# Kernel tuning notes

Measured on AMD Instinct MI355X. Metric: run time of the kernel, lower is better.

The kernel has to match this reference:

```python
import jax, jax.numpy as jnp
import numpy as np

N_EMBD = 1024
HEAD_SIZE = 128
B, T = 8, 2048


def apply_rope(x):
    # x: (B, T, D); rotate interleaved pairs, matching torch view(B,T,D//2,2)
    b, t, d = x.shape
    freqs = 1.0 / (10000.0 ** (jnp.arange(0, d, 2, dtype=jnp.float32) / d))  # (D//2,)
    angles = jnp.arange(t, dtype=jnp.float32)[:, None] * freqs[None, :]      # (T, D//2)
    cos_a = jnp.cos(angles).astype(x.dtype)
    sin_a = jnp.sin(angles).astype(x.dtype)
    xr = x.reshape(b, t, d // 2, 2)
    x0, x1 = xr[..., 0], xr[..., 1]
    rot = jnp.stack([x0 * cos_a - x1 * sin_a, x0 * sin_a + x1 * cos_a], axis=-1)
    return rot.reshape(b, t, d)


def setup_inputs() -> dict:
    key = jax.random.key(0)
    kx, kq, kk, kv = jax.random.split(key, 4)
    x = jax.random.normal(kx, (B, T, N_EMBD), dtype=jnp.float32)
    scale = 0.02
    Wq = jax.random.normal(kq, (N_EMBD, HEAD_SIZE), dtype=jnp.float32) * scale
    Wk = jax.random.normal(kk, (N_EMBD, HEAD_SIZE), dtype=jnp.float32) * scale
    Wv = jax.random.normal(kv, (N_EMBD, HEAD_SIZE), dtype=jnp.float32) * scale
    return {"x": x, "Wq": Wq, "Wk": Wk, "Wv": Wv}


def reference(x, Wq, Wk, Wv):
    # QKV projections (bias=False)
    q = x @ Wq  # (B, T, H)
    k = x @ Wk
    v = x @ Wv
    q = apply_rope(q)
    k = apply_rope(k)
    d = k.shape[-1]
    wei = jnp.einsum('bqd,bkd->bqk', q, k) * (d ** -0.5)  # (B, T, T)
    causal = jnp.tril(jnp.ones((q.shape[1], q.shape[1]), dtype=bool))
    wei = jnp.where(causal, wei, jnp.finfo(wei.dtype).min)
    wei = jax.nn.softmax(wei, axis=-1)
    out = jnp.einsum('bqk,bkd->bqd', wei, v)  # (B, T, H)
    return out
```

## Files before the change

kernel.cpp:

```cpp
#include <hip/hip_runtime.h>
#include <math.h>

#define BB 8
#define TT 2048
#define EE 1024
#define DD 128

typedef _Float16 f16x8 __attribute__((ext_vector_type(8)));
typedef _Float16 f16x4 __attribute__((ext_vector_type(4)));
typedef float    f32x4 __attribute__((ext_vector_type(4)));
typedef float    f32x16 __attribute__((ext_vector_type(16)));

#define QSCALE 0.12752406f

__global__ __launch_bounds__(256)
void wt_prep_kernel(const float* __restrict__ Wq,
                    const float* __restrict__ Wk,
                    const float* __restrict__ Wv,
                    _Float16* __restrict__ Wt)
{
    const int n = blockIdx.x;
    const int m = n >> 7;
    const float* __restrict__ W = (m == 0) ? Wq : (m == 1) ? Wk : Wv;
    const int nl = n & 127;
#pragma unroll
    for (int j = 0; j < 4; j++) {
        int kk = threadIdx.x + 256 * j;
        Wt[(size_t)n * EE + kk] = (_Float16)W[(size_t)kk * DD + nl];
    }
}

__global__ __launch_bounds__(512)
void proj_rope_kernel(const float* __restrict__ x,
                      const _Float16* __restrict__ Wt,
                      _Float16* __restrict__ qh,
                      _Float16* __restrict__ kh,
                      _Float16* __restrict__ vt)
{
    const int r0   = blockIdx.x * 64;
    const int tid  = threadIdx.x;
    const int wave = tid >> 6;
    const int lane = tid & 63;
    const int half = lane >> 5;
    const int col  = lane & 31;
    const int wave_m = wave & 1;
    const int wave_n = wave >> 1;

    __shared__ _Float16 Xs[64][72];
    __shared__ _Float16 Ws[384][72];
    __shared__ _Float16 Out[64][136];

    f32x16 acc[3];
#pragma unroll
    for (int s = 0; s < 3; s++) acc[s] = (f32x16)0.f;

    const int xrow = tid >> 3, xc8 = (tid & 7) * 8;

    float4 xa0, xa1;
    f16x8  wv[6];
    {
        const float* p = &x[(size_t)(r0 + xrow) * EE + xc8];
        xa0 = *(const float4*)p;
        xa1 = *(const float4*)(p + 4);
#pragma unroll
        for (int j = 0; j < 6; j++) {
            int ch = tid + 512 * j;
            int nn = ch >> 3, cw = (ch & 7) * 8;
            wv[j] = *(const f16x8*)&Wt[(size_t)nn * EE + cw];
        }
    }

    for (int it = 0; it < 16; it++) {
        __syncthreads();
        {
            f16x8 h = { (_Float16)xa0.x, (_Float16)xa0.y, (_Float16)xa0.z, (_Float16)xa0.w,
                        (_Float16)xa1.x, (_Float16)xa1.y, (_Float16)xa1.z, (_Float16)xa1.w };
            *(f16x8*)&Xs[xrow][xc8] = h;
#pragma unroll
            for (int j = 0; j < 6; j++) {
                int ch = tid + 512 * j;
                int nn = ch >> 3, cw = (ch & 7) * 8;
                *(f16x8*)&Ws[nn][cw] = wv[j];
            }
        }
        if (it + 1 < 16) {
            int k0 = (it + 1) * 64;
            const float* p = &x[(size_t)(r0 + xrow) * EE + k0 + xc8];
            xa0 = *(const float4*)p;
            xa1 = *(const float4*)(p + 4);
#pragma unroll
            for (int j = 0; j < 6; j++) {
                int ch = tid + 512 * j;
                int nn = ch >> 3, cw = (ch & 7) * 8;
                wv[j] = *(const f16x8*)&Wt[(size_t)nn * EE + k0 + cw];
            }
        }
        __syncthreads();
#pragma unroll
        for (int kc = 0; kc < 4; kc++) {
            f16x8 afr = *(f16x8*)&Xs[wave_m * 32 + col][kc * 16 + half * 8];
#pragma unroll
            for (int s = 0; s < 3; s++) {
                f16x8 bfr = *(f16x8*)&Ws[wave_n * 96 + s * 32 + col][kc * 16 + half * 8];
                acc[s] = __builtin_amdgcn_mfma_f32_32x32x16_f16(afr, bfr, acc[s], 0, 0, 0);
            }
        }
    }

    const int bidx = r0 >> 11;
    const int t0   = r0 & (TT - 1);

    for (int p = 0; p < 3; p++) {
        __syncthreads();
#pragma unroll
        for (int s = 0; s < 3; s++) {
            int gs = wave_n * 3 + s;
            if ((gs >> 2) != p) continue;
            int dcol = (gs & 3) * 32 + col;
            float f = 0.f;
            if (p < 2)
                f = __powf(10000.0f, -(float)(dcol & ~1) * (1.0f / 128.0f));
#pragma unroll
            for (int rg = 0; rg < 16; rg++) {
                int mrow = wave_m * 32 + (rg & 3) + 8 * (rg >> 2) + 4 * half;
                float av = acc[s][rg];
                float res;
                if (p < 2) {
                    float ap = __shfl_xor(av, 1);
                    float sa, ca;
                    __sincosf((float)(t0 + mrow) * f, &sa, &ca);
                    res = av * ca + ap * ((dcol & 1) ? sa : -sa);
                    if (p == 0) res *= QSCALE;
                } else {
                    res = av;
                }
                Out[mrow][dcol] = (_Float16)res;
            }
        }
        __syncthreads();
        if (p < 2) {
            _Float16* __restrict__ dst = ((p == 0) ? qh : kh) + (size_t)r0 * DD;
#pragma unroll
            for (int j = 0; j < 2; j++) {
                int cidx = tid + 512 * j;
                int row = cidx >> 4, o = cidx & 15;
                *(f16x8*)&dst[(size_t)row * DD + o * 8] = *(f16x8*)&Out[row][o * 8];
            }
        } else {
#pragma unroll
            for (int j = 0; j < 2; j++) {
                int u = tid + 512 * j;
                int d = u >> 3, tg = u & 7;
                f16x8 vv;
#pragma unroll
                for (int e = 0; e < 8; e++) vv[e] = Out[tg * 8 + e][d];
                *(f16x8*)&vt[((size_t)(bidx * DD + d)) * TT + t0 + tg * 8] = vv;
            }
        }
    }
}

__global__ __launch_bounds__(256)
void attn_kernel(const _Float16* __restrict__ qh,
                 const _Float16* __restrict__ kh,
                 const _Float16* __restrict__ vth,
                 _Float16* __restrict__ opart,
                 float* __restrict__ mpart,
                 float* __restrict__ lpart)
{
    const int b  = blockIdx.y;
    const int v_ = 39 - blockIdx.x;
    int xt, c;
    if (v_ < 4)       { xt = v_;                  c = 0; }
    else if (v_ < 12) { xt = 4 + ((v_ - 4) >> 1); c = (v_ - 4) & 1; }
    else if (v_ < 24) { xt = 8 + (v_ - 12) / 3;   c = (v_ - 12) % 3; }
    else              { xt = 12 + ((v_ - 24) >> 2); c = (v_ - 24) & 3; }
    const int q0 = xt * 128;
    const int nt = 2 * xt + 2;
    const int kt_begin = c * 8;
    const int kt_end   = (kt_begin + 8 < nt) ? (kt_begin + 8) : nt;

    const int tid  = threadIdx.x;
    const int wave = tid >> 6;
    const int lane = tid & 63;
    const int half = lane >> 5;
    const int col  = lane & 31;

    __shared__ _Float16 Ks[64][136];
    __shared__ _Float16 Vt[128][72];
    __shared__ _Float16 Ps[4][32][72];

    const int qg = q0 + wave * 32 + col;
    f16x8 qb[8];
#pragma unroll
    for (int kc = 0; kc < 8; kc++)
        qb[kc] = *(const f16x8*)&qh[((size_t)b * TT + qg) * DD + kc * 16 + half * 8];

    f32x16 Of[4];
#pragma unroll
    for (int t = 0; t < 4; t++) Of[t] = (f32x16)0.f;
    float m_ = -1e30f, l_ = 0.f;

    f16x8 kr[4], vr[4];
    {
        const int kb0 = kt_begin * 64;
#pragma unroll
        for (int i = 0; i < 4; i++) {
            int idx = i * 256 + tid;
            int key = idx >> 4, cc = idx & 15;
            kr[i] = *(const f16x8*)&kh[((size_t)b * TT + kb0 + key) * DD + cc * 8];
        }
#pragma unroll
        for (int i = 0; i < 4; i++) {
            int idx = i * 256 + tid;
            int d = idx >> 3, cc = idx & 7;
            vr[i] = *(const f16x8*)&vth[((size_t)b * DD + d) * TT + kb0 + cc * 8];
        }
    }

    for (int kt = kt_begin; kt < kt_end; kt++) {
        const int kb0 = kt * 64;
        __syncthreads();
#pragma unroll
        for (int i = 0; i < 4; i++) {
            int idx = i * 256 + tid;
            int key = idx >> 4, cc = idx & 15;
            *(f16x8*)&Ks[key][cc * 8] = kr[i];
        }
#pragma unroll
        for (int i = 0; i < 4; i++) {
            int idx = i * 256 + tid;
            int d = idx >> 3, cc = idx & 7;
            *(f16x8*)&Vt[d][cc * 8] = vr[i];
        }
        if (kt + 1 < kt_end) {
            const int kb1 = kb0 + 64;
#pragma unroll
            for (int i = 0; i < 4; i++) {
                int idx = i * 256 + tid;
                int key = idx >> 4, cc = idx & 15;
                kr[i] = *(const f16x8*)&kh[((size_t)b * TT + kb1 + key) * DD + cc * 8];
            }
#pragma unroll
            for (int i = 0; i < 4; i++) {
                int idx = i * 256 + tid;
                int d = idx >> 3, cc = idx & 7;
                vr[i] = *(const f16x8*)&vth[((size_t)b * DD + d) * TT + kb1 + cc * 8];
            }
        }
        __syncthreads();

        f32x16 sf[2];
#pragma unroll
        for (int g = 0; g < 2; g++) {
            sf[g] = (f32x16)0.f;
#pragma unroll
            for (int kc = 0; kc < 8; kc++) {
                f16x8 kf = *(f16x8*)&Ks[g * 32 + col][kc * 16 + half * 8];
                sf[g] = __builtin_amdgcn_mfma_f32_32x32x16_f16(kf, qb[kc], sf[g], 0, 0, 0);
            }
        }

        const bool diag = (kt >= 2 * xt);
        float mloc = -1e30f;
#pragma unroll
        for (int g = 0; g < 2; g++)
#pragma unroll
            for (int rg = 0; rg < 16; rg++) {
                int key = kb0 + g * 32 + (rg & 3) + 8 * (rg >> 2) + 4 * half;
                float val = sf[g][rg];
                val = (!diag || key <= qg) ? val : -1e30f;
                sf[g][rg] = val;
                mloc = fmaxf(mloc, val);
            }
        mloc = fmaxf(mloc, __shfl_xor(mloc, 32));
        float mnew  = fmaxf(m_, mloc);
        float alpha = __builtin_amdgcn_exp2f(m_ - mnew);
        float ps = 0.f;
#pragma unroll
        for (int g = 0; g < 2; g++) {
#pragma unroll
            for (int rc = 0; rc < 4; rc++) {
                f16x4 p4;
#pragma unroll
                for (int rr = 0; rr < 4; rr++) {
                    float p = __builtin_amdgcn_exp2f(sf[g][4 * rc + rr] - mnew);
                    ps += p;
                    p4[rr] = (_Float16)p;
                }
                *(f16x4*)&Ps[wave][col][g * 32 + 8 * rc + 4 * half] = p4;
            }
        }
        ps += __shfl_xor(ps, 32);
        l_ = l_ * alpha + ps;
        m_ = mnew;
#pragma unroll
        for (int t = 0; t < 4; t++) Of[t] *= alpha;

        f16x8 pb[4];
#pragma unroll
        for (int kc = 0; kc < 4; kc++)
            pb[kc] = *(f16x8*)&Ps[wave][col][kc * 16 + half * 8];
#pragma unroll
        for (int t = 0; t < 4; t++) {
#pragma unroll
            for (int kc = 0; kc < 4; kc++) {
                f16x8 vf = *(f16x8*)&Vt[t * 32 + col][kc * 16 + half * 8];
                Of[t] = __builtin_amdgcn_mfma_f32_32x32x16_f16(vf, pb[kc], Of[t], 0, 0, 0);
            }
        }
    }

    const int slot = (b * 16 + xt) * 4 + c;
    _Float16* op = opart + ((size_t)slot * 128 + wave * 32 + col) * DD;
#pragma unroll
    for (int t = 0; t < 4; t++) {
#pragma unroll
        for (int rc = 0; rc < 4; rc++) {
            f16x4 o4 = { (_Float16)Of[t][4 * rc + 0], (_Float16)Of[t][4 * rc + 1],
                         (_Float16)Of[t][4 * rc + 2], (_Float16)Of[t][4 * rc + 3] };
            *(f16x4*)&op[t * 32 + 8 * rc + 4 * half] = o4;
        }
    }
    if (half == 0) {
        mpart[slot * 128 + wave * 32 + col] = m_;
        lpart[slot * 128 + wave * 32 + col] = l_;
    }
}

__global__ __launch_bounds__(256)
void combine_kernel(const _Float16* __restrict__ opart,
                    const float* __restrict__ mpart,
                    const float* __restrict__ lpart,
                    float* __restrict__ out)
{
    int gid = blockIdx.x * 256 + threadIdx.x;
    int d   = gid & 127;
    int t   = gid >> 7;
    int b   = t >> 11;
    int tl  = t & (TT - 1);
    int xt  = tl >> 7;
    int rl  = tl & 127;
    int np  = (2 * xt + 2 + 7) >> 3;
    int sb  = (b * 16 + xt) * 4;

    float mm = -1e30f;
    for (int j = 0; j < np; j++)
        mm = fmaxf(mm, mpart[(sb + j) * 128 + rl]);
    float acc = 0.f, den = 0.f;
    for (int j = 0; j < np; j++) {
        float w = __builtin_amdgcn_exp2f(mpart[(sb + j) * 128 + rl] - mm);
        den += w * lpart[(sb + j) * 128 + rl];
        acc += w * (float)opart[((size_t)(sb + j) * 128 + rl) * DD + d];
    }
    out[gid] = acc / den;
}

extern "C" void kernel_launch(void* const* d_in, const int* in_sizes, int n_in,
                              void* d_out, int out_size, void* d_ws, size_t ws_size,
                              hipStream_t stream)
{
    const float* x  = (const float*)d_in[0];
    const float* Wq = (const float*)d_in[1];
    const float* Wk = (const float*)d_in[2];
    const float* Wv = (const float*)d_in[3];
    float* out = (float*)d_out;

    const size_t NTOK = (size_t)BB * TT;
    _Float16* qh = (_Float16*)d_ws;
    _Float16* kh = qh + NTOK * DD;
    _Float16* vt = kh + NTOK * DD;
    _Float16* Wt = vt + NTOK * DD;
    _Float16* opart = Wt + (size_t)384 * EE;
    float* mp = (float*)(opart + (size_t)512 * 128 * DD);
    float* lp = mp + 512 * 128;

    wt_prep_kernel<<<dim3(384), dim3(256), 0, stream>>>(Wq, Wk, Wv, Wt);
    proj_rope_kernel<<<dim3(256), dim3(512), 0, stream>>>(x, Wt, qh, kh, vt);
    attn_kernel<<<dim3(40, BB), dim3(256), 0, stream>>>(qh, kh, vt, opart, mp, lp);
    combine_kernel<<<dim3((int)(NTOK * DD / 256)), dim3(256), 0, stream>>>(opart, mp, lp, out);
}
```

Baseline: 184.5 us.

## Pre-swizzle Q/K/V and weights into MFMA fragment order, drop LDS staging

Weights, Q, K and V are written in a layout that matches the MFMA operand fragments, so each lane can load its f16x8 fragment straight from global memory. This removes the shared-memory tiles and their barriers in both the projection and attention kernels. The cost is that K/V reuse across the 4 waves now depends on L1/L2 cache instead of LDS, with more global load traffic per block. Register prefetch pipelining is also gone, so load latency may be exposed.

```diff
diff --git a/kernel.cpp b/kernel.cpp
--- a/kernel.cpp
+++ b/kernel.cpp
@@ -13,29 +13,35 @@
 
 #define QSCALE 0.12752406f
 
+
 __global__ __launch_bounds__(256)
 void wt_prep_kernel(const float* __restrict__ Wq,
                     const float* __restrict__ Wk,
                     const float* __restrict__ Wv,
-                    _Float16* __restrict__ Wt)
-{
-    const int n = blockIdx.x;
-    const int m = n >> 7;
-    const float* __restrict__ W = (m == 0) ? Wq : (m == 1) ? Wk : Wv;
-    const int nl = n & 127;
-#pragma unroll
-    for (int j = 0; j < 4; j++) {
-        int kk = threadIdx.x + 256 * j;
-        Wt[(size_t)n * EE + kk] = (_Float16)W[(size_t)kk * DD + nl];
-    }
+                    _Float16* __restrict__ Wb)
+{
+    int gid = blockIdx.x * 256 + threadIdx.x;
+    int kc  = gid / 768;
+    int rem = gid - kc * 768;
+    int ns  = rem >> 6;
+    int ln  = rem & 63;
+    int n   = ns * 32 + (ln & 31);
+    int k0  = kc * 16 + (ln >> 5) * 8;
+    const float* __restrict__ W = (n < 128) ? Wq : (n < 256) ? Wk : Wv;
+    int nl = n & 127;
+    f16x8 w;
+#pragma unroll
+    for (int j = 0; j < 8; j++)
+        w[j] = (_Float16)W[(size_t)(k0 + j) * DD + nl];
+    *(f16x8*)&Wb[(size_t)gid * 8] = w;
 }
 
 __global__ __launch_bounds__(512)
 void proj_rope_kernel(const float* __restrict__ x,
-                      const _Float16* __restrict__ Wt,
-                      _Float16* __restrict__ qh,
-                      _Float16* __restrict__ kh,
-                      _Float16* __restrict__ vt)
+                      const _Float16* __restrict__ Wb,
+                      _Float16* __restrict__ Qb,
+                      _Float16* __restrict__ Ka,
+                      _Float16* __restrict__ Va)
 {
     const int r0   = blockIdx.x * 64;
     const int tid  = threadIdx.x;
@@ -46,64 +52,25 @@
     const int wave_m = wave & 1;
     const int wave_n = wave >> 1;
 
-    __shared__ _Float16 Xs[64][72];
-    __shared__ _Float16 Ws[384][72];
     __shared__ _Float16 Out[64][136];
 
     f32x16 acc[3];
 #pragma unroll
     for (int s = 0; s < 3; s++) acc[s] = (f32x16)0.f;
 
-    const int xrow = tid >> 3, xc8 = (tid & 7) * 8;
-
-    float4 xa0, xa1;
-    f16x8  wv[6];
-    {
-        const float* p = &x[(size_t)(r0 + xrow) * EE + xc8];
-        xa0 = *(const float4*)p;
-        xa1 = *(const float4*)(p + 4);
-#pragma unroll
-        for (int j = 0; j < 6; j++) {
-            int ch = tid + 512 * j;
-            int nn = ch >> 3, cw = (ch & 7) * 8;
-            wv[j] = *(const f16x8*)&Wt[(size_t)nn * EE + cw];
-        }
-    }
-
-    for (int it = 0; it < 16; it++) {
-        __syncthreads();
-        {
-            f16x8 h = { (_Float16)xa0.x, (_Float16)xa0.y, (_Float16)xa0.z, (_Float16)xa0.w,
-                        (_Float16)xa1.x, (_Float16)xa1.y, (_Float16)xa1.z, (_Float16)xa1.w };
-            *(f16x8*)&Xs[xrow][xc8] = h;
-#pragma unroll
-            for (int j = 0; j < 6; j++) {
-                int ch = tid + 512 * j;
-                int nn = ch >> 3, cw = (ch & 7) * 8;
-                *(f16x8*)&Ws[nn][cw] = wv[j];
-            }
-        }
-        if (it + 1 < 16) {
-            int k0 = (it + 1) * 64;
-            const float* p = &x[(size_t)(r0 + xrow) * EE + k0 + xc8];
-            xa0 = *(const float4*)p;
-            xa1 = *(const float4*)(p + 4);
-#pragma unroll
-            for (int j = 0; j < 6; j++) {
-                int ch = tid + 512 * j;
-                int nn = ch >> 3, cw = (ch & 7) * 8;
-                wv[j] = *(const f16x8*)&Wt[(size_t)nn * EE + k0 + cw];
-            }
-        }
-        __syncthreads();
-#pragma unroll
-        for (int kc = 0; kc < 4; kc++) {
-            f16x8 afr = *(f16x8*)&Xs[wave_m * 32 + col][kc * 16 + half * 8];
-#pragma unroll
-            for (int s = 0; s < 3; s++) {
-                f16x8 bfr = *(f16x8*)&Ws[wave_n * 96 + s * 32 + col][kc * 16 + half * 8];
-                acc[s] = __builtin_amdgcn_mfma_f32_32x32x16_f16(afr, bfr, acc[s], 0, 0, 0);
-            }
+    const float* __restrict__ xp =
+        &x[(size_t)(r0 + wave_m * 32 + col) * EE + half * 8];
+
+#pragma unroll 4
+    for (int kc = 0; kc < 64; kc++) {
+        float4 a0 = *(const float4*)(xp + kc * 16);
+        float4 a1 = *(const float4*)(xp + kc * 16 + 4);
+        f16x8 afr = { (_Float16)a0.x, (_Float16)a0.y, (_Float16)a0.z, (_Float16)a0.w,
+                      (_Float16)a1.x, (_Float16)a1.y, (_Float16)a1.z, (_Float16)a1.w };
+#pragma unroll
+        for (int s = 0; s < 3; s++) {
+            f16x8 bfr = *(const f16x8*)&Wb[((size_t)kc * 12 + wave_n * 3 + s) * 512 + lane * 8];
+            acc[s] = __builtin_amdgcn_mfma_f32_32x32x16_f16(afr, bfr, acc[s], 0, 0, 0);
         }
     }
 
@@ -139,31 +106,35 @@
         }
         __syncthreads();
         if (p < 2) {
-            _Float16* __restrict__ dst = ((p == 0) ? qh : kh) + (size_t)r0 * DD;
-#pragma unroll
-            for (int j = 0; j < 2; j++) {
-                int cidx = tid + 512 * j;
-                int row = cidx >> 4, o = cidx & 15;
-                *(f16x8*)&dst[(size_t)row * DD + o * 8] = *(f16x8*)&Out[row][o * 8];
+            _Float16* __restrict__ dst = (p == 0) ? Qb : Ka;
+#pragma unroll
+            for (int jj = 0; jj < 2; jj++) {
+                int cid = tid + 512 * jj;
+                int sl = cid >> 9, kc = (cid >> 6) & 7, ln = cid & 63;
+                f16x8 v8 = *(f16x8*)&Out[sl * 32 + (ln & 31)][kc * 16 + (ln >> 5) * 8];
+                size_t ga = ((((size_t)bidx * 64 + (t0 >> 5) + sl) * 8 + kc) * 64 + ln) * 8;
+                *(f16x8*)&dst[ga] = v8;
             }
         } else {
 #pragma unroll
-            for (int j = 0; j < 2; j++) {
-                int u = tid + 512 * j;
-                int d = u >> 3, tg = u & 7;
+            for (int jj = 0; jj < 2; jj++) {
+                int cid = tid + 512 * jj;
+                int kcl = cid >> 8, ds = (cid >> 6) & 3, ln = cid & 63;
                 f16x8 vv;
 #pragma unroll
-                for (int e = 0; e < 8; e++) vv[e] = Out[tg * 8 + e][d];
-                *(f16x8*)&vt[((size_t)(bidx * DD + d)) * TT + t0 + tg * 8] = vv;
+                for (int e = 0; e < 8; e++)
+                    vv[e] = Out[kcl * 16 + (ln >> 5) * 8 + e][ds * 32 + (ln & 31)];
+                size_t ga = ((((size_t)bidx * 128 + (t0 >> 4) + kcl) * 4 + ds) * 64 + ln) * 8;
+                *(f16x8*)&Va[ga] = vv;
             }
         }
     }
 }
 
 __global__ __launch_bounds__(256)
-void attn_kernel(const _Float16* __restrict__ qh,
-                 const _Float16* __restrict__ kh,
-                 const _Float16* __restrict__ vth,
+void attn_kernel(const _Float16* __restrict__ Qb,
+                 const _Float16* __restrict__ Ka,
+                 const _Float16* __restrict__ Va,
                  _Float16* __restrict__ opart,
                  float* __restrict__ mpart,
                  float* __restrict__ lpart)
@@ -186,69 +157,21 @@
     const int half = lane >> 5;
     const int col  = lane & 31;
 
-    __shared__ _Float16 Ks[64][136];
-    __shared__ _Float16 Vt[128][72];
     __shared__ _Float16 Ps[4][32][72];
 
     const int qg = q0 + wave * 32 + col;
     f16x8 qb[8];
 #pragma unroll
     for (int kc = 0; kc < 8; kc++)
-        qb[kc] = *(const f16x8*)&qh[((size_t)b * TT + qg) * DD + kc * 16 + half * 8];
+        qb[kc] = *(const f16x8*)&Qb[((((size_t)b * 64 + xt * 4 + wave) * 8 + kc) * 64 + lane) * 8];
 
     f32x16 Of[4];
 #pragma unroll
     for (int t = 0; t < 4; t++) Of[t] = (f32x16)0.f;
     float m_ = -1e30f, l_ = 0.f;
 
-    f16x8 kr[4], vr[4];
-    {
-        const int kb0 = kt_begin * 64;
-#pragma unroll
-        for (int i = 0; i < 4; i++) {
-            int idx = i * 256 + tid;
-            int key = idx >> 4, cc = idx & 15;
-            kr[i] = *(const f16x8*)&kh[((size_t)b * TT + kb0 + key) * DD + cc * 8];
-        }
-#pragma unroll
-        for (int i = 0; i < 4; i++) {
-            int idx = i * 256 + tid;
-            int d = idx >> 3, cc = idx & 7;
-            vr[i] = *(const f16x8*)&vth[((size_t)b * DD + d) * TT + kb0 + cc * 8];
-        }
-    }
-
     for (int kt = kt_begin; kt < kt_end; kt++) {
         const int kb0 = kt * 64;
-        __syncthreads();
-#pragma unroll
-        for (int i = 0; i < 4; i++) {
-            int idx = i * 256 + tid;
-            int key = idx >> 4, cc = idx & 15;
-            *(f16x8*)&Ks[key][cc * 8] = kr[i];
-        }
-#pragma unroll
-        for (int i = 0; i < 4; i++) {
-            int idx = i * 256 + tid;
-            int d = idx >> 3, cc = idx & 7;
-            *(f16x8*)&Vt[d][cc * 8] = vr[i];
-        }
-        if (kt + 1 < kt_end) {
-            const int kb1 = kb0 + 64;
-#pragma unroll
-            for (int i = 0; i < 4; i++) {
-                int idx = i * 256 + tid;
-                int key = idx >> 4, cc = idx & 15;
-                kr[i] = *(const f16x8*)&kh[((size_t)b * TT + kb1 + key) * DD + cc * 8];
-            }
-#pragma unroll
-            for (int i = 0; i < 4; i++) {
-                int idx = i * 256 + tid;
-                int d = idx >> 3, cc = idx & 7;
-                vr[i] = *(const f16x8*)&vth[((size_t)b * DD + d) * TT + kb1 + cc * 8];
-            }
-        }
-        __syncthreads();
 
         f32x16 sf[2];
 #pragma unroll
@@ -256,7 +179,7 @@
             sf[g] = (f32x16)0.f;
 #pragma unroll
             for (int kc = 0; kc < 8; kc++) {
-                f16x8 kf = *(f16x8*)&Ks[g * 32 + col][kc * 16 + half * 8];
+                f16x8 kf = *(const f16x8*)&Ka[((((size_t)b * 64 + 2 * kt + g) * 8 + kc) * 64 + lane) * 8];
                 sf[g] = __builtin_amdgcn_mfma_f32_32x32x16_f16(kf, qb[kc], sf[g], 0, 0, 0);
             }
         }
@@ -304,9 +227,9 @@
 #pragma unroll
         for (int t = 0; t < 4; t++) {
 #pragma unroll
-            for (int kc = 0; kc < 4; kc++) {
-                f16x8 vf = *(f16x8*)&Vt[t * 32 + col][kc * 16 + half * 8];
-                Of[t] = __builtin_amdgcn_mfma_f32_32x32x16_f16(vf, pb[kc], Of[t], 0, 0, 0);
+            for (int kcl = 0; kcl < 4; kcl++) {
+                f16x8 vf = *(const f16x8*)&Va[((((size_t)b * 128 + kt * 4 + kcl) * 4 + t) * 64 + lane) * 8];
+                Of[t] = __builtin_amdgcn_mfma_f32_32x32x16_f16(vf, pb[kcl], Of[t], 0, 0, 0);
             }
         }
     }
@@ -367,16 +290,16 @@
     float* out = (float*)d_out;
 
     const size_t NTOK = (size_t)BB * TT;
-    _Float16* qh = (_Float16*)d_ws;
-    _Float16* kh = qh + NTOK * DD;
-    _Float16* vt = kh + NTOK * DD;
-    _Float16* Wt = vt + NTOK * DD;
-    _Float16* opart = Wt + (size_t)384 * EE;
+    _Float16* Qb = (_Float16*)d_ws;
+    _Float16* Ka = Qb + NTOK * DD;
+    _Float16* Va = Ka + NTOK * DD;
+    _Float16* Wb = Va + NTOK * DD;
+    _Float16* opart = Wb + (size_t)384 * EE;
     float* mp = (float*)(opart + (size_t)512 * 128 * DD);
     float* lp = mp + 512 * 128;
 
-    wt_prep_kernel<<<dim3(384), dim3(256), 0, stream>>>(Wq, Wk, Wv, Wt);
-    proj_rope_kernel<<<dim3(256), dim3(512), 0, stream>>>(x, Wt, qh, kh, vt);
-    attn_kernel<<<dim3(40, BB), dim3(256), 0, stream>>>(qh, kh, vt, opart, mp, lp);
+    wt_prep_kernel<<<dim3(192), dim3(256), 0, stream>>>(Wq, Wk, Wv, Wb);
+    proj_rope_kernel<<<dim3(256), dim3(512), 0, stream>>>(x, Wb, Qb, Ka, Va);
+    attn_kernel<<<dim3(40, BB), dim3(256), 0, stream>>>(Qb, Ka, Va, opart, mp, lp);
     combine_kernel<<<dim3((int)(NTOK * DD / 256)), dim3(256), 0, stream>>>(opart, mp, lp, out);
 }
```

After: 194.5 us. 5.4% more time.
